# Kernel tuning notes

Measured on AMD Instinct MI355X. Metric: run time of the kernel, lower is better.

The kernel has to match this reference:

```python
import jax, jax.numpy as jnp
import numpy as np
import math

EMBED_DIM = 1024
NUM_HEADS = 16
B, S = 4, 4096
NEG_INF = -1e30


def setup_inputs() -> dict:
    key = jax.random.key(0)
    k1, k2, k3, k4 = jax.random.split(key, 4)
    D = EMBED_DIM
    # xavier_uniform bounds
    lim_in = math.sqrt(6.0 / (3 * D + D))
    lim_out = math.sqrt(6.0 / (D + D))
    return {
        "x": jax.random.normal(k1, (B, S, D), dtype=jnp.float32),
        "in_proj_weight": jax.random.uniform(k2, (3 * D, D), dtype=jnp.float32, minval=-lim_in, maxval=lim_in),
        "in_proj_bias": jnp.zeros((3 * D,), dtype=jnp.float32),
        "out_proj_weight": jax.random.uniform(k3, (D, D), dtype=jnp.float32, minval=-lim_out, maxval=lim_out),
        "out_proj_bias": jnp.zeros((D,), dtype=jnp.float32),
    }


def _cron_root_attention(q, k, v):
    """Causal sqrt(N) block-sparse attention.

    q,k,v: [B, H, S, hd]. Sequence split into nb blocks of size b = sqrt(S).
    Each query attends to: (a) keys in its own block (causal within block),
    (b) one summary key per strictly-previous block (the block's last key).
    Complexity O(S * (b + nb)) = O(N * sqrt(N)).
    """
    Bq, H, Sq, hd = q.shape
    b = int(round(math.sqrt(Sq)))
    nb = Sq // b
    scale = 1.0 / math.sqrt(hd)

    qb = q.reshape(Bq, H, nb, b, hd)
    kb = k.reshape(Bq, H, nb, b, hd)
    vb = v.reshape(Bq, H, nb, b, hd)
    ks = k[:, :, b - 1::b, :]  # [B, H, nb, hd] summary keys (last of each block)
    vs = v[:, :, b - 1::b, :]

    # local (within-block) scores, causal mask
    s_loc = jnp.einsum("bhnqd,bhnkd->bhnqk", qb, kb) * scale  # [B,H,nb,b,b]
    idx = jnp.arange(b)
    loc_mask = idx[:, None] >= idx[None, :]  # [b, b]
    s_loc = jnp.where(loc_mask[None, None, None], s_loc, NEG_INF)

    # strided scores to summary keys of strictly previous blocks
    s_str = jnp.einsum("bhnqd,bhmd->bhnqm", qb, ks) * scale  # [B,H,nb,b,nb]
    nidx = jnp.arange(nb)
    str_mask = nidx[:, None] > nidx[None, :]  # [nb(query block), nb(key block)]
    s_str = jnp.where(str_mask[None, None, :, None, :], s_str, NEG_INF)

    # joint softmax over local + strided keys
    scores = jnp.concatenate([s_loc, s_str], axis=-1)  # [B,H,nb,b,b+nb]
    w = jax.nn.softmax(scores, axis=-1)
    w_loc, w_str = w[..., :b], w[..., b:]

    out = jnp.einsum("bhnqk,bhnkd->bhnqd", w_loc, vb) \
        + jnp.einsum("bhnqm,bhmd->bhnqd", w_str, vs)
    return out.reshape(Bq, H, Sq, hd)


def reference(x, in_proj_weight, in_proj_bias, out_proj_weight, out_proj_bias):
    Bx, Sx, D = x.shape
    H = NUM_HEADS
    hd = D // H
    qkv = x @ in_proj_weight.T + in_proj_bias  # [B,S,3D]
    qkv = jnp.transpose(qkv.reshape(Bx, Sx, 3, H, hd), (2, 0, 3, 1, 4))
    q, k, v = qkv[0], qkv[1], qkv[2]  # each [B,H,S,hd]
    out = _cron_root_attention(q, k, v)  # [B,H,S,hd]
    out = jnp.transpose(out, (0, 2, 1, 3)).reshape(Bx, Sx, D)
    return out @ out_proj_weight.T + out_proj_bias
```

## Files before the change

### kernel.cpp

```cpp
#include <hip/hip_runtime.h>
#include <stdint.h>

typedef __attribute__((ext_vector_type(8))) short short8;
typedef __attribute__((ext_vector_type(4))) float f32x4;
typedef __attribute__((ext_vector_type(4))) float f4;
typedef __attribute__((ext_vector_type(4))) ushort us4;

#define AS1 __attribute__((address_space(1)))
#define AS3 __attribute__((address_space(3)))

__device__ __forceinline__ ushort f2bf(float f) {
  uint u = __builtin_bit_cast(uint, f);
  u += 0x7fffu + ((u >> 16) & 1u);
  return (ushort)(u >> 16);
}

__global__ void cvt_bf16(const float* __restrict__ in, ushort* __restrict__ out, int n4) {
  int i = blockIdx.x * blockDim.x + threadIdx.x;
  int stride = gridDim.x * blockDim.x;
  for (; i < n4; i += stride) {
    f4 v = ((const f4*)in)[i];
    us4 o;
    o[0] = f2bf(v[0]); o[1] = f2bf(v[1]); o[2] = f2bf(v[2]); o[3] = f2bf(v[3]);
    ((us4*)out)[i] = o;
  }
}


__device__ __forceinline__ void stage_half(const ushort* __restrict__ g, int pitch,
                                           int row0, int k0, char* ldsbase, int tid) {
#pragma unroll
  for (int i = 0; i < 2; ++i) {
    uint chunk = i * 512 + tid;
    uint Q = chunk << 4;
    uint L = Q ^ (((Q >> 7) & 7u) << 4);
    uint row = L >> 7;
    uint kb = L & 127u;
    const char* gp = (const char*)(g + (size_t)(row0 + (int)row) * pitch + k0) + kb;
    char* lp = ldsbase + ((i * 512 + (tid & ~63)) << 4);
    __builtin_amdgcn_global_load_lds((const AS1 void*)gp, (AS3 void*)lp, 16, 0, 0);
  }
}

__device__ __forceinline__ void stage_j(int j, const ushort* __restrict__ A,
                                        const ushort* __restrict__ Bw, int K,
                                        int arow0, int brow0, char* sA, char* sB, int tid) {
  int t = j >> 2, h = j & 3;
  int k0 = t << 6;
  char* base = ((h < 2) ? sB : sA) + ((t & 1) << 15) + ((h & 1) << 14);
  const ushort* g = (h < 2) ? Bw : A;
  int row0 = ((h < 2) ? brow0 : arow0) + ((h & 1) << 7);
  stage_half(g, K, row0, k0, base, tid);
}

template <int OUT_F32>
__global__ __launch_bounds__(512, 1) void gemm256(const ushort* __restrict__ A,
                                                  const ushort* __restrict__ Bw,
                                                  const float* __restrict__ bias,
                                                  void* __restrict__ Cout,
                                                  int M, int N, int K, int gn) {
  __shared__ char sA[65536];
  __shared__ char sB[65536];
  const int tid = threadIdx.x;
  const int lane = tid & 63, l15 = lane & 15, lk = lane >> 4;
  const int w = tid >> 6;
  const int wm = w >> 2, wn = w & 3;
  const int NT = K >> 6;

  int q8 = gridDim.x >> 3;
  int bid = blockIdx.x;
  int swz = (bid & 7) * q8 + (bid >> 3);
  int bm = swz / gn, bn = swz % gn;
  const int arow0 = bm << 8, brow0 = bn << 8;

  f32x4 acc[8][4];
  f32x4 zero = {0.f, 0.f, 0.f, 0.f};
#pragma unroll
  for (int i = 0; i < 8; ++i)
#pragma unroll
    for (int j = 0; j < 4; ++j) acc[i][j] = zero;

#pragma unroll
  for (int j = 0; j < 7; ++j)
    if (j < 4 * NT) stage_j(j, A, Bw, K, arow0, brow0, sA, sB, tid);
  asm volatile("s_waitcnt vmcnt(6)" ::: "memory");
  __builtin_amdgcn_s_barrier();

  for (int t = 0; t < NT; ++t) {
    const char* bA = sA + ((t & 1) << 15);
    const char* bB = sB + ((t & 1) << 15);
    short8 bfr[4][2];
#pragma unroll
    for (int qd = 0; qd < 4; ++qd) {
      short8 afr[2][2];
      if (qd == 0) {
#pragma unroll
        for (int ni = 0; ni < 4; ++ni)
#pragma unroll
          for (int kk = 0; kk < 2; ++kk) {
            uint row = (uint)(wn * 64 + ni * 16 + l15);
            uint byte = (row << 7) + (kk << 6) + (lk << 4);
            bfr[ni][kk] = *(const short8*)&bB[byte ^ ((row & 7u) << 4)];
          }
      }
#pragma unroll
      for (int mi = 0; mi < 2; ++mi)
#pragma unroll
        for (int kk = 0; kk < 2; ++kk) {
          uint row = (uint)(wm * 128 + (qd * 2 + mi) * 16 + l15);
          uint byte = (row << 7) + (kk << 6) + (lk << 4);
          afr[mi][kk] = *(const short8*)&bA[byte ^ ((row & 7u) << 4)];
        }
      int j = 4 * t + qd + 7;
      if (j < 4 * NT) stage_j(j, A, Bw, K, arow0, brow0, sA, sB, tid);
      if (qd == 3) {
        if (t < NT - 2) asm volatile("s_waitcnt vmcnt(6)" ::: "memory");
        else if (t == NT - 2) asm volatile("s_waitcnt vmcnt(0)" ::: "memory");
      }
      __builtin_amdgcn_s_barrier();
      asm volatile("s_waitcnt lgkmcnt(0)" ::: "memory");
      __builtin_amdgcn_s_setprio(1);
#pragma unroll
      for (int kk = 0; kk < 2; ++kk)
#pragma unroll
        for (int mi = 0; mi < 2; ++mi)
#pragma unroll
          for (int ni = 0; ni < 4; ++ni)
            acc[qd * 2 + mi][ni] = __builtin_amdgcn_mfma_f32_16x16x32_bf16(
                afr[mi][kk], bfr[ni][kk], acc[qd * 2 + mi][ni], 0, 0, 0);
      __builtin_amdgcn_s_setprio(0);
      __builtin_amdgcn_s_barrier();
    }
  }

#pragma unroll
  for (int m = 0; m < 8; ++m)
#pragma unroll
    for (int ni = 0; ni < 4; ++ni)
#pragma unroll
      for (int r = 0; r < 4; ++r) {
        int row = arow0 + wm * 128 + m * 16 + lk * 4 + r;
        int col = brow0 + wn * 64 + ni * 16 + l15;
        float v = acc[m][ni][r] + bias[col];
        if constexpr (OUT_F32)
          ((float*)Cout)[(size_t)row * N + col] = v;
        else
          ((ushort*)Cout)[(size_t)row * N + col] = f2bf(v);
      }
}

__global__ __launch_bounds__(256) void cron_attn(const ushort* __restrict__ qkv,
                                                 ushort* __restrict__ aout) {
  const int S = 4096, CQ = 3072;
  int bid = blockIdx.x;
  int n = bid & 63;
  int h = (bid >> 6) & 15;
  int b = bid >> 10;
  int tid = threadIdx.x;
  int w = tid >> 6, lane = tid & 63, l15 = lane & 15, lk = lane >> 4;

  const ushort* qp = qkv + (size_t)b * S * CQ + h * 64;
  const ushort* kp = qp + 1024;
  const ushort* vp = qp + 2048;

  __shared__ char vT[16384];
  __shared__ char pL[4][4096];

  {
    int r = tid >> 1;
    int half = tid & 1;
    int srow = (r < 64) ? (n * 64 + r) : ((r - 64) * 64 + 63);
    const ushort* src = vp + (size_t)srow * CQ + half * 32;
    short8 vv0 = ((const short8*)src)[0];
    short8 vv1 = ((const short8*)src)[1];
    short8 vv2 = ((const short8*)src)[2];
    short8 vv3 = ((const short8*)src)[3];
#pragma unroll
    for (int j = 0; j < 8; ++j) {
      int d0 = half * 32 + j;
      *(short*)&vT[(uint)(d0 * 256 + r * 2) ^ (((uint)d0 & 7u) << 4)] = vv0[j];
      int d1 = half * 32 + 8 + j;
      *(short*)&vT[(uint)(d1 * 256 + r * 2) ^ (((uint)d1 & 7u) << 4)] = vv1[j];
      int d2 = half * 32 + 16 + j;
      *(short*)&vT[(uint)(d2 * 256 + r * 2) ^ (((uint)d2 & 7u) << 4)] = vv2[j];
      int d3 = half * 32 + 24 + j;
      *(short*)&vT[(uint)(d3 * 256 + r * 2) ^ (((uint)d3 & 7u) << 4)] = vv3[j];
    }
  }
  __syncthreads();

  short8 aq[2];
  {
    int srow = n * 64 + w * 16 + l15;
#pragma unroll
    for (int kk = 0; kk < 2; ++kk)
      aq[kk] = *(const short8*)(qp + (size_t)srow * CQ + kk * 32 + lk * 8);
  }

  f32x4 sc[8];
  f32x4 zero = {0.f, 0.f, 0.f, 0.f};
#pragma unroll
  for (int c = 0; c < 8; ++c) sc[c] = zero;
#pragma unroll
  for (int c = 0; c < 8; ++c) {
    int key = (c < 4) ? (n * 64 + c * 16 + l15) : (((c - 4) * 16 + l15) * 64 + 63);
    const ushort* kr = kp + (size_t)key * CQ;
#pragma unroll
    for (int kk = 0; kk < 2; ++kk) {
      short8 bk = *(const short8*)(kr + kk * 32 + lk * 8);
      sc[c] = __builtin_amdgcn_mfma_f32_16x16x32_bf16(aq[kk], bk, sc[c], 0, 0, 0);
    }
  }

  float p[8][4];
  int qrow = w * 16 + lk * 4;
#pragma unroll
  for (int c = 0; c < 8; ++c)
#pragma unroll
    for (int r = 0; r < 4; ++r) {
      float s = sc[c][r] * 0.125f;
      bool ok = (c < 4) ? ((qrow + r) >= (c * 16 + l15)) : (((c - 4) * 16 + l15) < n);
      p[c][r] = ok ? s : -1e30f;
    }

#pragma unroll
  for (int r = 0; r < 4; ++r) {
    float m = p[0][r];
#pragma unroll
    for (int c = 1; c < 8; ++c) m = fmaxf(m, p[c][r]);
    m = fmaxf(m, __shfl_xor(m, 1));
    m = fmaxf(m, __shfl_xor(m, 2));
    m = fmaxf(m, __shfl_xor(m, 4));
    m = fmaxf(m, __shfl_xor(m, 8));
    float sum = 0.f;
#pragma unroll
    for (int c = 0; c < 8; ++c) {
      p[c][r] = __expf(p[c][r] - m);
      sum += p[c][r];
    }
    sum += __shfl_xor(sum, 1);
    sum += __shfl_xor(sum, 2);
    sum += __shfl_xor(sum, 4);
    sum += __shfl_xor(sum, 8);
    float rs = 1.f / sum;
#pragma unroll
    for (int c = 0; c < 8; ++c) p[c][r] *= rs;
  }

  char* myP = pL[w];
#pragma unroll
  for (int c = 0; c < 8; ++c)
#pragma unroll
    for (int r = 0; r < 4; ++r) {
      uint row = lk * 4 + r;
      uint byte = row * 256 + (c * 16 + l15) * 2;
      *(short*)&myP[byte ^ ((row & 7u) << 4)] = (short)f2bf(p[c][r]);
    }
  short8 ap[4];
#pragma unroll
  for (int kk = 0; kk < 4; ++kk) {
    uint row = (uint)l15;
    uint byte = row * 256 + (kk * 32 + lk * 8) * 2;
    ap[kk] = *(const short8*)&myP[byte ^ ((row & 7u) << 4)];
  }

  f32x4 ao[4];
#pragma unroll
  for (int dc = 0; dc < 4; ++dc) ao[dc] = zero;
#pragma unroll
  for (int dc = 0; dc < 4; ++dc)
#pragma unroll
    for (int kk = 0; kk < 4; ++kk) {
      uint d = dc * 16 + l15;
      uint byte = d * 256 + (kk * 32 + lk * 8) * 2;
      short8 bv = *(const short8*)&vT[byte ^ ((d & 7u) << 4)];
      ao[dc] = __builtin_amdgcn_mfma_f32_16x16x32_bf16(ap[kk], bv, ao[dc], 0, 0, 0);
    }

#pragma unroll
  for (int dc = 0; dc < 4; ++dc)
#pragma unroll
    for (int r = 0; r < 4; ++r) {
      int srow = n * 64 + w * 16 + lk * 4 + r;
      int col = h * 64 + dc * 16 + l15;
      aout[((size_t)(b * S + srow)) * 1024 + col] = f2bf(ao[dc][r]);
    }
}

extern "C" void kernel_launch(void* const* d_in, const int* in_sizes, int n_in,
                              void* d_out, int out_size, void* d_ws, size_t ws_size,
                              hipStream_t stream) {
  const float* x = (const float*)d_in[0];
  const float* wi = (const float*)d_in[1];
  const float* bi = (const float*)d_in[2];
  const float* wo = (const float*)d_in[3];
  const float* bo = (const float*)d_in[4];
  float* out = (float*)d_out;
  char* ws = (char*)d_ws;

  ushort* xb = (ushort*)(ws);
  ushort* wib = (ushort*)(ws + (size_t)33554432);
  ushort* wob = (ushort*)(ws + (size_t)39845888);
  ushort* qkvb = (ushort*)(ws + (size_t)41943040);
  ushort* aob = (ushort*)(ws + (size_t)142606336);

  cvt_bf16<<<2048, 256, 0, stream>>>(x, xb, (16384 * 1024) / 4);
  cvt_bf16<<<768, 256, 0, stream>>>(wi, wib, (3072 * 1024) / 4);
  cvt_bf16<<<256, 256, 0, stream>>>(wo, wob, (1024 * 1024) / 4);

  gemm256<0><<<64 * 12, 512, 0, stream>>>(xb, wib, bi, qkvb, 16384, 3072, 1024, 12);
  cron_attn<<<4096, 256, 0, stream>>>(qkvb, aob);
  gemm256<1><<<64 * 4, 512, 0, stream>>>(aob, wob, bo, out, 16384, 1024, 1024, 4);
}
```

Before: 225.1 us.

## Prefetch GEMM LDS fragments one quarter ahead and fuse bf16 converts

```diff
diff --git a/kernel.cpp b/kernel.cpp
--- a/kernel.cpp
+++ b/kernel.cpp
@@ -15,14 +15,30 @@
   return (ushort)(u >> 16);
 }
 
-__global__ void cvt_bf16(const float* __restrict__ in, ushort* __restrict__ out, int n4) {
+__global__ void cvt_all(const float* __restrict__ x, const float* __restrict__ wi,
+                        const float* __restrict__ wo, ushort* __restrict__ xb,
+                        ushort* __restrict__ wib, ushort* __restrict__ wob) {
+  const int n_x = (16384 * 1024) / 4;
+  const int n_wi = (3072 * 1024) / 4;
+  const int n_wo = (1024 * 1024) / 4;
+  const int n_tot = n_x + n_wi + n_wo;
   int i = blockIdx.x * blockDim.x + threadIdx.x;
   int stride = gridDim.x * blockDim.x;
-  for (; i < n4; i += stride) {
-    f4 v = ((const f4*)in)[i];
+  for (; i < n_tot; i += stride) {
+    const float* src;
+    ushort* dst;
+    int idx;
+    if (i < n_x) {
+      src = x; dst = xb; idx = i;
+    } else if (i < n_x + n_wi) {
+      src = wi; dst = wib; idx = i - n_x;
+    } else {
+      src = wo; dst = wob; idx = i - n_x - n_wi;
+    }
+    f4 v = ((const f4*)src)[idx];
     us4 o;
     o[0] = f2bf(v[0]); o[1] = f2bf(v[1]); o[2] = f2bf(v[2]); o[3] = f2bf(v[3]);
-    ((us4*)out)[i] = o;
+    ((us4*)dst)[idx] = o;
   }
 }
 
@@ -53,8 +69,30 @@
   stage_half(g, K, row0, k0, base, tid);
 }
 
+#define LOAD_A(set, tt, qq)                                                     \
+  {                                                                             \
+    const char* bA_ = sA + (((tt) & 1) << 15);                                  \
+    _Pragma("unroll") for (int mi = 0; mi < 2; ++mi) _Pragma("unroll")          \
+        for (int kk = 0; kk < 2; ++kk) {                                        \
+      uint row = (uint)(wm * 128 + ((qq) * 2 + mi) * 16 + l15);                 \
+      uint byte = (row << 7) + (kk << 6) + (lk << 4);                           \
+      afr[set][mi][kk] = *(const short8*)&bA_[byte ^ ((row & 7u) << 4)];        \
+    }                                                                           \
+  }
+
+#define LOAD_B(tt)                                                              \
+  {                                                                             \
+    const char* bB_ = sB + (((tt) & 1) << 15);                                  \
+    _Pragma("unroll") for (int ni = 0; ni < 4; ++ni) _Pragma("unroll")          \
+        for (int kk = 0; kk < 2; ++kk) {                                        \
+      uint row = (uint)(wn * 64 + ni * 16 + l15);                               \
+      uint byte = (row << 7) + (kk << 6) + (lk << 4);                           \
+      bfr[ni][kk] = *(const short8*)&bB_[byte ^ ((row & 7u) << 4)];             \
+    }                                                                           \
+  }
+
 template <int OUT_F32>
-__global__ __launch_bounds__(512, 1) void gemm256(const ushort* __restrict__ A,
+__global__ __launch_bounds__(512, 2) void gemm256(const ushort* __restrict__ A,
                                                   const ushort* __restrict__ Bw,
                                                   const float* __restrict__ bias,
                                                   void* __restrict__ Cout,
@@ -80,37 +118,19 @@
 #pragma unroll
     for (int j = 0; j < 4; ++j) acc[i][j] = zero;
 
-#pragma unroll
-  for (int j = 0; j < 7; ++j)
-    if (j < 4 * NT) stage_j(j, A, Bw, K, arow0, brow0, sA, sB, tid);
+  short8 afr[2][2][2];
+  short8 bfr[4][2];
+
+#pragma unroll
+  for (int j = 0; j < 7; ++j) stage_j(j, A, Bw, K, arow0, brow0, sA, sB, tid);
   asm volatile("s_waitcnt vmcnt(6)" ::: "memory");
   __builtin_amdgcn_s_barrier();
+  asm volatile("" ::: "memory");
+  LOAD_A(0, 0, 0);
 
   for (int t = 0; t < NT; ++t) {
-    const char* bA = sA + ((t & 1) << 15);
-    const char* bB = sB + ((t & 1) << 15);
-    short8 bfr[4][2];
 #pragma unroll
     for (int qd = 0; qd < 4; ++qd) {
-      short8 afr[2][2];
-      if (qd == 0) {
-#pragma unroll
-        for (int ni = 0; ni < 4; ++ni)
-#pragma unroll
-          for (int kk = 0; kk < 2; ++kk) {
-            uint row = (uint)(wn * 64 + ni * 16 + l15);
-            uint byte = (row << 7) + (kk << 6) + (lk << 4);
-            bfr[ni][kk] = *(const short8*)&bB[byte ^ ((row & 7u) << 4)];
-          }
-      }
-#pragma unroll
-      for (int mi = 0; mi < 2; ++mi)
-#pragma unroll
-        for (int kk = 0; kk < 2; ++kk) {
-          uint row = (uint)(wm * 128 + (qd * 2 + mi) * 16 + l15);
-          uint byte = (row << 7) + (kk << 6) + (lk << 4);
-          afr[mi][kk] = *(const short8*)&bA[byte ^ ((row & 7u) << 4)];
-        }
       int j = 4 * t + qd + 7;
       if (j < 4 * NT) stage_j(j, A, Bw, K, arow0, brow0, sA, sB, tid);
       if (qd == 3) {
@@ -118,7 +138,15 @@
         else if (t == NT - 2) asm volatile("s_waitcnt vmcnt(0)" ::: "memory");
       }
       __builtin_amdgcn_s_barrier();
-      asm volatile("s_waitcnt lgkmcnt(0)" ::: "memory");
+      asm volatile("" ::: "memory");
+      if (qd == 0) LOAD_B(t);
+      if (qd == 0) LOAD_A(1, t, 1);
+      if (qd == 1) LOAD_A(0, t, 2);
+      if (qd == 2) LOAD_A(1, t, 3);
+      if (qd == 3) {
+        if (t < NT - 1) LOAD_A(0, t + 1, 0);
+      }
+      __builtin_amdgcn_sched_barrier(0);
       __builtin_amdgcn_s_setprio(1);
 #pragma unroll
       for (int kk = 0; kk < 2; ++kk)
@@ -127,7 +155,7 @@
 #pragma unroll
           for (int ni = 0; ni < 4; ++ni)
             acc[qd * 2 + mi][ni] = __builtin_amdgcn_mfma_f32_16x16x32_bf16(
-                afr[mi][kk], bfr[ni][kk], acc[qd * 2 + mi][ni], 0, 0, 0);
+                afr[qd & 1][mi][kk], bfr[ni][kk], acc[qd * 2 + mi][ni], 0, 0, 0);
       __builtin_amdgcn_s_setprio(0);
       __builtin_amdgcn_s_barrier();
     }
@@ -304,9 +332,7 @@
   ushort* qkvb = (ushort*)(ws + (size_t)41943040);
   ushort* aob = (ushort*)(ws + (size_t)142606336);
 
-  cvt_bf16<<<2048, 256, 0, stream>>>(x, xb, (16384 * 1024) / 4);
-  cvt_bf16<<<768, 256, 0, stream>>>(wi, wib, (3072 * 1024) / 4);
-  cvt_bf16<<<256, 256, 0, stream>>>(wo, wob, (1024 * 1024) / 4);
+  cvt_all<<<2048, 256, 0, stream>>>(x, wi, wo, xb, wib, wob);
 
   gemm256<0><<<64 * 12, 512, 0, stream>>>(xb, wib, bi, qkvb, 16384, 3072, 1024, 12);
   cron_attn<<<4096, 256, 0, stream>>>(qkvb, aob);
```

Result: slower. 238.0 us (+5.8%).
